# Kernel optimization log

Hardware: AMD Instinct MI355X
Metric: run time of the kernel (lower is better)

## Reference

```python
import jax, jax.numpy as jnp
import numpy as np

DIM = 256
HEADS = 8
WIN = 64
SHIFT = 32
HIDDEN = 1024  # dim * mlp_ratio
EPS = 1e-5


def layernorm(x, g, b):
    mu = jnp.mean(x, axis=-1, keepdims=True)
    var = jnp.mean(jnp.square(x - mu), axis=-1, keepdims=True)
    return (x - mu) * jax.lax.rsqrt(var + EPS) * g + b


def setup_inputs() -> dict:
    key = jax.random.key(0)
    ks = jax.random.split(key, 12)
    B, L = 8, 16384
    s = lambda fan: 1.0 / np.sqrt(fan)
    return {
        "x": jax.random.normal(ks[0], (B, L, DIM), dtype=jnp.float32),
        "g1": jnp.ones((DIM,), jnp.float32),
        "b1": jnp.zeros((DIM,), jnp.float32),
        "qkv_w": jax.random.normal(ks[1], (DIM, 3 * DIM), jnp.float32) * s(DIM),
        "qkv_b": jnp.zeros((3 * DIM,), jnp.float32),
        "rpb_table": jax.random.normal(ks[2], (2 * WIN - 1, HEADS), jnp.float32) * 0.02,
        "proj_w": jax.random.normal(ks[3], (DIM, DIM), jnp.float32) * s(DIM),
        "proj_b": jnp.zeros((DIM,), jnp.float32),
        "g2": jnp.ones((DIM,), jnp.float32),
        "b2": jnp.zeros((DIM,), jnp.float32),
        "fc1_w": jax.random.normal(ks[4], (DIM, HIDDEN), jnp.float32) * s(DIM),
        "fc1_b": jnp.zeros((HIDDEN,), jnp.float32),
        "fc2_w": jax.random.normal(ks[5], (HIDDEN, DIM), jnp.float32) * s(HIDDEN),
        "fc2_b": jnp.zeros((DIM,), jnp.float32),
    }


def reference(x, g1, b1, qkv_w, qkv_b, rpb_table, proj_w, proj_b, g2, b2, fc1_w, fc1_b, fc2_w, fc2_b):
    B, L, C = x.shape
    hd = C // HEADS
    scale = hd ** (-0.5)

    shortcut = x
    xn = layernorm(x, g1, b1)

    # shift: roll left, zero wrapped-around tail (faithful to original in-place zeroing)
    shifted = jnp.roll(xn, -SHIFT, axis=1)
    shifted = shifted.at[:, -SHIFT:].set(0.0)

    nW = L // WIN
    xw = shifted.reshape(B * nW, WIN, C)

    # qkv projection
    qkv = xw @ qkv_w + qkv_b
    qkv = qkv.reshape(-1, WIN, 3, HEADS, hd).transpose(2, 0, 3, 1, 4)
    q, k, v = qkv[0], qkv[1], qkv[2]

    attn = jnp.einsum('bhnd,bhmd->bhnm', q * scale, k)

    idx = jnp.arange(WIN)
    rel = idx[:, None] - idx[None, :] + (WIN - 1)
    bias = rpb_table[rel].transpose(2, 0, 1)
    attn = attn + bias[None]

    attn = jax.nn.softmax(attn, axis=-1)
    out = jnp.einsum('bhnm,bhmd->bhnd', attn, v)
    out = out.transpose(0, 2, 1, 3).reshape(-1, WIN, C)
    out = out @ proj_w + proj_b

    # window reverse + unshift (zero wrapped head, faithful to original)
    xr = out.reshape(B, L, C)
    xr = jnp.roll(xr, SHIFT, axis=1)
    xr = xr.at[:, :SHIFT].set(0.0)

    x1 = shortcut + xr
    h = layernorm(x1, g2, b2)
    h = jax.nn.gelu(h @ fc1_w + fc1_b, approximate=False)
    h = h @ fc2_w + fc2_b
    return x1 + h
```

## Files before the change

### kernel.cpp

```cpp
#include <hip/hip_runtime.h>
#include <hip/hip_bf16.h>
#include <stdint.h>

#define LSEQ   16384
#define NBATCH 8
#define MROWS  (NBATCH*LSEQ)
#define CDIM   256
#define NHEADS 8
#define HDIM   32
#define NWIN   64
#define NSH    32
#define NHID   1024

typedef unsigned short u16;
typedef __attribute__((ext_vector_type(4))) float f32x4;
typedef __attribute__((ext_vector_type(8))) short s16x8;

__device__ __forceinline__ u16 f2bf(float f) {
  union { float f; unsigned u; } c; c.f = f;
  unsigned r = c.u + 0x7FFFu + ((c.u >> 16) & 1u);
  return (u16)(r >> 16);
}

__device__ __forceinline__ float gelu_fast(float v) {
  float t = v * v;
  float u2 = v * fmaf(t, 0.0713548162726f, 1.59576912161f);
  float e = __expf(u2);
  float r = __builtin_amdgcn_rcpf(e + 1.f);
  return fmaf(-v, r, v);
}

__global__ __launch_bounds__(256) void wtrans_kernel(const float* __restrict__ in,
                                                     u16* __restrict__ out, int K, int N) {
  __shared__ float tile[64][65];
  int k0 = blockIdx.x * 64, n0 = blockIdx.y * 64;
  int t = threadIdx.x;
  int r = t >> 4, cb = (t & 15) * 4;
#pragma unroll
  for (int p = 0; p < 4; ++p) {
    const float4 v = *(const float4*)(in + (size_t)(k0 + r + p*16) * N + n0 + cb);
    tile[r+p*16][cb+0] = v.x; tile[r+p*16][cb+1] = v.y;
    tile[r+p*16][cb+2] = v.z; tile[r+p*16][cb+3] = v.w;
  }
  __syncthreads();
#pragma unroll
  for (int p = 0; p < 4; ++p) {
    int nl = r + p*16;
    ushort4 o;
    o.x = f2bf(tile[cb+0][nl]); o.y = f2bf(tile[cb+1][nl]);
    o.z = f2bf(tile[cb+2][nl]); o.w = f2bf(tile[cb+3][nl]);
    *(ushort4*)(out + (size_t)(n0+nl)*K + k0 + cb) = o;
  }
}

__global__ __launch_bounds__(256) void ln_shift_kernel(const float* __restrict__ x,
                                                       const float* __restrict__ g,
                                                       const float* __restrict__ b,
                                                       u16* __restrict__ out) {
  int row  = blockIdx.x * 4 + (threadIdx.x >> 6);
  int lane = threadIdx.x & 63;
  u16* op = out + (size_t)row * CDIM + lane*4;
  int l  = row & (LSEQ-1);
  int ls = l + NSH;
  if (ls >= LSEQ) { *(ushort4*)op = make_ushort4(0,0,0,0); return; }
  const float4 v = *(const float4*)(x + ((size_t)(row - l) + ls) * CDIM + lane*4);
  float s  = v.x+v.y+v.z+v.w;
  float s2 = v.x*v.x + v.y*v.y + v.z*v.z + v.w*v.w;
#pragma unroll
  for (int m = 1; m < 64; m <<= 1) { s += __shfl_xor(s, m); s2 += __shfl_xor(s2, m); }
  float mean = s * (1.f/CDIM);
  float rs = rsqrtf(s2*(1.f/CDIM) - mean*mean + 1e-5f);
  const float4 gv = *(const float4*)(g + lane*4);
  const float4 bv = *(const float4*)(b + lane*4);
  ushort4 o;
  o.x = f2bf((v.x-mean)*rs*gv.x + bv.x);
  o.y = f2bf((v.y-mean)*rs*gv.y + bv.y);
  o.z = f2bf((v.z-mean)*rs*gv.z + bv.z);
  o.w = f2bf((v.w-mean)*rs*gv.w + bv.w);
  *(ushort4*)op = o;
}

__global__ __launch_bounds__(256) void ln2_kernel(const float* __restrict__ x,
                                                  float* __restrict__ x1,
                                                  const float* __restrict__ g,
                                                  const float* __restrict__ b,
                                                  u16* __restrict__ out) {
  int row  = blockIdx.x * 4 + (threadIdx.x >> 6);
  int lane = threadIdx.x & 63;
  int l = row & (LSEQ-1);
  float* dp = x1 + (size_t)row * CDIM + lane*4;
  float4 v;
  if (l < NSH) { v = *(const float4*)(x + (size_t)row * CDIM + lane*4); *(float4*)dp = v; }
  else         { v = *(const float4*)dp; }
  float s  = v.x+v.y+v.z+v.w;
  float s2 = v.x*v.x + v.y*v.y + v.z*v.z + v.w*v.w;
#pragma unroll
  for (int m = 1; m < 64; m <<= 1) { s += __shfl_xor(s, m); s2 += __shfl_xor(s2, m); }
  float mean = s * (1.f/CDIM);
  float rs = rsqrtf(s2*(1.f/CDIM) - mean*mean + 1e-5f);
  const float4 gv = *(const float4*)(g + lane*4);
  const float4 bv = *(const float4*)(b + lane*4);
  ushort4 o;
  o.x = f2bf((v.x-mean)*rs*gv.x + bv.x);
  o.y = f2bf((v.y-mean)*rs*gv.y + bv.y);
  o.z = f2bf((v.z-mean)*rs*gv.z + bv.z);
  o.w = f2bf((v.w-mean)*rs*gv.w + bv.w);
  *(ushort4*)(out + (size_t)row * CDIM + lane*4) = o;
}

template<int KDIM, int NDIM, int EPI>
__global__ __launch_bounds__(256) void gemm_kernel(const u16* __restrict__ A,
                                                   const u16* __restrict__ BT,
                                                   const float* __restrict__ bias,
                                                   void* __restrict__ Cout,
                                                   const float* __restrict__ res) {
  __shared__ __align__(16) u16 As[128*64];
  __shared__ __align__(16) u16 Bs[128*64];
  const int t = threadIdx.x, wave = t >> 6, lane = t & 63;
  constexpr int NT_N = NDIM / 128;
  constexpr int G = 32;
  const int bid = blockIdx.x;
  const int chunk = bid / (G * NT_N);
  const int rem = bid - chunk * (G * NT_N);
  const int tn = rem / G;
  const int tm = chunk * G + (rem - tn * G);
  f32x4 acc[4][4];
#pragma unroll
  for (int m = 0; m < 4; ++m)
#pragma unroll
    for (int n = 0; n < 4; ++n) acc[m][n] = (f32x4){0.f,0.f,0.f,0.f};

  const size_t Aoff = (size_t)tm * 128 * KDIM;
  const size_t Boff = (size_t)tn * 128 * KDIM;
  int rowS[4], kblkS[4];
#pragma unroll
  for (int p = 0; p < 4; ++p) {
    int i = p*256 + t; rowS[p] = i >> 3;
    kblkS[p] = ((i & 7) ^ (rowS[p] & 7)) * 8;
  }
  const int wr = (wave >> 1) * 64, wc = (wave & 1) * 64;

  for (int kt = 0; kt < KDIM/64; ++kt) {
    const int k0 = kt * 64;
#pragma unroll
    for (int p = 0; p < 4; ++p) {
      __builtin_amdgcn_global_load_lds(
        (const __attribute__((address_space(1))) void*)(A + Aoff + (size_t)rowS[p]*KDIM + k0 + kblkS[p]),
        (__attribute__((address_space(3))) void*)(As + (p*256 + wave*64)*8), 16, 0, 0);
      __builtin_amdgcn_global_load_lds(
        (const __attribute__((address_space(1))) void*)(BT + Boff + (size_t)rowS[p]*KDIM + k0 + kblkS[p]),
        (__attribute__((address_space(3))) void*)(Bs + (p*256 + wave*64)*8), 16, 0, 0);
    }
    asm volatile("s_waitcnt vmcnt(0)" ::: "memory");
    __syncthreads();
#pragma unroll
    for (int kk = 0; kk < 2; ++kk) {
      s16x8 af[4], bf[4];
#pragma unroll
      for (int m = 0; m < 4; ++m) {
        int r = wr + m*16 + (lane & 15);
        int slot = (kk*4 + (lane >> 4)) ^ (r & 7);
        af[m] = *(const s16x8*)&As[r*64 + slot*8];
      }
#pragma unroll
      for (int n = 0; n < 4; ++n) {
        int r = wc + n*16 + (lane & 15);
        int slot = (kk*4 + (lane >> 4)) ^ (r & 7);
        bf[n] = *(const s16x8*)&Bs[r*64 + slot*8];
      }
#pragma unroll
      for (int m = 0; m < 4; ++m)
#pragma unroll
        for (int n = 0; n < 4; ++n)
          acc[m][n] = __builtin_amdgcn_mfma_f32_16x16x32_bf16(bf[n], af[m], acc[m][n], 0, 0, 0);
    }
    __syncthreads();
  }

  const int g = lane >> 4, c0 = lane & 15;
  const size_t row0 = (size_t)tm*128 + wr;
  const int col0 = tn*128 + wc;
  float4 bvv[4];
#pragma unroll
  for (int n = 0; n < 4; ++n) bvv[n] = *(const float4*)(bias + col0 + n*16 + g*4);

  if constexpr (EPI == 0) {
    u16* out = (u16*)Cout;
#pragma unroll
    for (int m = 0; m < 4; ++m) {
      size_t R = row0 + m*16 + c0;
      u16* orow = out + R * NDIM + col0 + g*4;
#pragma unroll
      for (int n = 0; n < 4; ++n) {
        ushort4 o;
        o.x = f2bf(acc[m][n][0] + bvv[n].x);
        o.y = f2bf(acc[m][n][1] + bvv[n].y);
        o.z = f2bf(acc[m][n][2] + bvv[n].z);
        o.w = f2bf(acc[m][n][3] + bvv[n].w);
        *(ushort4*)(orow + n*16) = o;
      }
    }
  } else if constexpr (EPI == 1) {
    float* out = (float*)Cout;
#pragma unroll
    for (int m = 0; m < 4; ++m) {
      size_t R = row0 + m*16 + c0;
      int l = (int)(R & (LSEQ-1));
      if (l < LSEQ - NSH) {
        size_t base = (R + NSH) * CDIM + col0 + g*4;
#pragma unroll
        for (int n = 0; n < 4; ++n) {
          float4 rv = *(const float4*)(res + base + n*16);
          float4 o;
          o.x = rv.x + acc[m][n][0] + bvv[n].x;
          o.y = rv.y + acc[m][n][1] + bvv[n].y;
          o.z = rv.z + acc[m][n][2] + bvv[n].z;
          o.w = rv.w + acc[m][n][3] + bvv[n].w;
          *(float4*)(out + base + n*16) = o;
        }
      }
    }
  } else if constexpr (EPI == 2) {
    u16* out = (u16*)Cout;
#pragma unroll
    for (int m = 0; m < 4; ++m) {
      size_t R = row0 + m*16 + c0;
      u16* orow = out + R * NDIM + col0 + g*4;
#pragma unroll
      for (int n = 0; n < 4; ++n) {
        ushort4 o;
        o.x = f2bf(gelu_fast(acc[m][n][0] + bvv[n].x));
        o.y = f2bf(gelu_fast(acc[m][n][1] + bvv[n].y));
        o.z = f2bf(gelu_fast(acc[m][n][2] + bvv[n].z));
        o.w = f2bf(gelu_fast(acc[m][n][3] + bvv[n].w));
        *(ushort4*)(orow + n*16) = o;
      }
    }
  } else {
    float* out = (float*)Cout;
#pragma unroll
    for (int m = 0; m < 4; ++m) {
      size_t R = row0 + m*16 + c0;
      size_t base = R * NDIM + col0 + g*4;
#pragma unroll
      for (int n = 0; n < 4; ++n) {
        float4 rv = *(const float4*)(res + base + n*16);
        float4 o;
        o.x = rv.x + acc[m][n][0] + bvv[n].x;
        o.y = rv.y + acc[m][n][1] + bvv[n].y;
        o.z = rv.z + acc[m][n][2] + bvv[n].z;
        o.w = rv.w + acc[m][n][3] + bvv[n].w;
        *(float4*)(out + base + n*16) = o;
      }
    }
  }
}

__global__ __launch_bounds__(256) void attn_kernel(const u16* __restrict__ qkv,
                                                   const float* __restrict__ rpb,
                                                   u16* __restrict__ out) {
  __shared__ __align__(16) u16 VT[NHEADS*HDIM*NWIN];
  __shared__ __align__(16) u16 Pl[4*NWIN*NWIN];
  __shared__ float biasl[NHEADS][128];
  const int t = threadIdx.x, wave = t >> 6, lane = t & 63;
  const int g = lane >> 4, c0 = lane & 15;
  const size_t rowbase = (size_t)blockIdx.x * NWIN;

  for (int e = t; e < NHEADS*128; e += 256) {
    int h = e >> 7, i = e & 127;
    biasl[h][i] = (i < 2*NWIN-1) ? rpb[i*NHEADS + h] : 0.f;
  }
  {
    int cA = t >> 5;
    int inner = t & 31;
    int hh = inner >> 2, d0 = (inner & 3) * 8;
#pragma unroll
    for (int p = 0; p < 8; ++p) {
      int c = p*8 + cA;
      s16x8 v = *(const s16x8*)&qkv[(rowbase + c)*768 + 512 + hh*32 + d0];
#pragma unroll
      for (int j = 0; j < 8; ++j) {
        int d = d0 + j;
        int slot = (c >> 3) ^ (d & 7) ^ hh;
        *(u16*)((char*)VT + hh*4096 + d*128 + slot*16 + (c & 7)*2) = (u16)v[j];
      }
    }
  }
  __syncthreads();

  const float scale = 0.17677669529663687f;
#pragma unroll 1
  for (int rep = 0; rep < 2; ++rep) {
    const int h = wave*2 + rep;
    s16x8 qf[4], kf[4];
#pragma unroll
    for (int m = 0; m < 4; ++m)
      qf[m] = *(const s16x8*)&qkv[(rowbase + m*16 + c0)*768 + h*32 + g*8];
#pragma unroll
    for (int n = 0; n < 4; ++n)
      kf[n] = *(const s16x8*)&qkv[(rowbase + n*16 + c0)*768 + 256 + h*32 + g*8];
    f32x4 sa[4][4];
#pragma unroll
    for (int m = 0; m < 4; ++m)
#pragma unroll
      for (int n = 0; n < 4; ++n) sa[m][n] = (f32x4){0.f,0.f,0.f,0.f};
#pragma unroll
    for (int m = 0; m < 4; ++m)
#pragma unroll
      for (int n = 0; n < 4; ++n)
        sa[m][n] = __builtin_amdgcn_mfma_f32_16x16x32_bf16(qf[m], kf[n], sa[m][n], 0, 0, 0);
#pragma unroll
    for (int m = 0; m < 4; ++m)
#pragma unroll
      for (int n = 0; n < 4; ++n) {
        int idx0 = (m-n)*16 + 4*g - c0 + 63;
#pragma unroll
        for (int j = 0; j < 4; ++j)
          sa[m][n][j] = sa[m][n][j]*scale + biasl[h][idx0 + j];
      }
    float rm[4][4], rsum[4][4];
#pragma unroll
    for (int m = 0; m < 4; ++m)
#pragma unroll
      for (int j = 0; j < 4; ++j) {
        float mx = fmaxf(fmaxf(sa[m][0][j], sa[m][1][j]), fmaxf(sa[m][2][j], sa[m][3][j]));
        mx = fmaxf(mx, __shfl_xor(mx, 1));
        mx = fmaxf(mx, __shfl_xor(mx, 2));
        mx = fmaxf(mx, __shfl_xor(mx, 4));
        mx = fmaxf(mx, __shfl_xor(mx, 8));
        rm[m][j] = mx;
      }
#pragma unroll
    for (int m = 0; m < 4; ++m)
#pragma unroll
      for (int n = 0; n < 4; ++n)
#pragma unroll
        for (int j = 0; j < 4; ++j)
          sa[m][n][j] = __expf(sa[m][n][j] - rm[m][j]);
#pragma unroll
    for (int m = 0; m < 4; ++m)
#pragma unroll
      for (int j = 0; j < 4; ++j) {
        float s = sa[m][0][j] + sa[m][1][j] + sa[m][2][j] + sa[m][3][j];
        s += __shfl_xor(s, 1);
        s += __shfl_xor(s, 2);
        s += __shfl_xor(s, 4);
        s += __shfl_xor(s, 8);
        rsum[m][j] = 1.f / s;
      }
    asm volatile("s_waitcnt lgkmcnt(0)" ::: "memory");
#pragma unroll
    for (int m = 0; m < 4; ++m)
#pragma unroll
      for (int n = 0; n < 4; ++n)
#pragma unroll
        for (int j = 0; j < 4; ++j) {
          int r = m*16 + 4*g + j, c = n*16 + c0;
          *(u16*)((char*)Pl + wave*8192 + r*128 + (((c>>3)^(r&7))*16) + (c&7)*2)
            = f2bf(sa[m][n][j] * rsum[m][j]);
        }
    asm volatile("s_waitcnt lgkmcnt(0)" ::: "memory");
    __builtin_amdgcn_sched_barrier(0);
    f32x4 oa[4][2];
#pragma unroll
    for (int m = 0; m < 4; ++m) { oa[m][0] = (f32x4){0.f,0.f,0.f,0.f}; oa[m][1] = (f32x4){0.f,0.f,0.f,0.f}; }
#pragma unroll
    for (int kk = 0; kk < 2; ++kk) {
      s16x8 pa[4], vb[2];
#pragma unroll
      for (int m = 0; m < 4; ++m) {
        int r = m*16 + c0;
        int slot = (kk*4 + g) ^ (r & 7);
        pa[m] = *(const s16x8*)((const char*)Pl + wave*8192 + r*128 + slot*16);
      }
#pragma unroll
      for (int n = 0; n < 2; ++n) {
        int d = n*16 + c0;
        int slot = (kk*4 + g) ^ (d & 7) ^ h;
        vb[n] = *(const s16x8*)((const char*)VT + h*4096 + d*128 + slot*16);
      }
#pragma unroll
      for (int m = 0; m < 4; ++m)
#pragma unroll
        for (int n = 0; n < 2; ++n)
          oa[m][n] = __builtin_amdgcn_mfma_f32_16x16x32_bf16(vb[n], pa[m], oa[m][n], 0, 0, 0);
    }
#pragma unroll
    for (int m = 0; m < 4; ++m) {
      u16* op = out + (rowbase + m*16 + c0)*CDIM + h*32 + g*4;
#pragma unroll
      for (int n = 0; n < 2; ++n) {
        ushort4 o;
        o.x = f2bf(oa[m][n][0]); o.y = f2bf(oa[m][n][1]);
        o.z = f2bf(oa[m][n][2]); o.w = f2bf(oa[m][n][3]);
        *(ushort4*)(op + n*16) = o;
      }
    }
  }
}

extern "C" void kernel_launch(void* const* d_in, const int* in_sizes, int n_in,
                              void* d_out, int out_size, void* d_ws, size_t ws_size,
                              hipStream_t stream) {
  const float* x      = (const float*)d_in[0];
  const float* g1     = (const float*)d_in[1];
  const float* b1     = (const float*)d_in[2];
  const float* qkv_w  = (const float*)d_in[3];
  const float* qkv_b  = (const float*)d_in[4];
  const float* rpb    = (const float*)d_in[5];
  const float* proj_w = (const float*)d_in[6];
  const float* proj_b = (const float*)d_in[7];
  const float* g2     = (const float*)d_in[8];
  const float* b2     = (const float*)d_in[9];
  const float* fc1_w  = (const float*)d_in[10];
  const float* fc1_b  = (const float*)d_in[11];
  const float* fc2_w  = (const float*)d_in[12];
  const float* fc2_b  = (const float*)d_in[13];
  float* out = (float*)d_out;

  u16* R0     = (u16*)d_ws;
  u16* R1     = R0 + (size_t)MROWS*768;
  u16* qkvwT  = R1 + (size_t)MROWS*1024;
  u16* projwT = qkvwT + 768*256;
  u16* fc1wT  = projwT + 256*256;
  u16* fc2wT  = fc1wT + 1024*256;

  wtrans_kernel<<<dim3(4, 12), 256, 0, stream>>>(qkv_w, qkvwT, 256, 768);
  wtrans_kernel<<<dim3(4, 4),  256, 0, stream>>>(proj_w, projwT, 256, 256);
  wtrans_kernel<<<dim3(4, 16), 256, 0, stream>>>(fc1_w, fc1wT, 256, 1024);
  wtrans_kernel<<<dim3(16, 4), 256, 0, stream>>>(fc2_w, fc2wT, 1024, 256);

  constexpr int NT_M = MROWS/128;
  ln_shift_kernel<<<MROWS/4, 256, 0, stream>>>(x, g1, b1, R1);
  gemm_kernel<256, 768, 0><<<NT_M*6, 256, 0, stream>>>(R1, qkvwT, qkv_b, R0, nullptr);
  attn_kernel<<<MROWS/NWIN, 256, 0, stream>>>(R0, rpb, R1);
  gemm_kernel<256, 256, 1><<<NT_M*2, 256, 0, stream>>>(R1, projwT, proj_b, out, x);
  ln2_kernel<<<MROWS/4, 256, 0, stream>>>(x, out, g2, b2, R0);
  gemm_kernel<256, 1024, 2><<<NT_M*8, 256, 0, stream>>>(R0, fc1wT, fc1_b, R1, nullptr);
  gemm_kernel<1024, 256, 3><<<NT_M*2, 256, 0, stream>>>(R1, fc2wT, fc2_b, out, out);
}
```

Before: 669.0 us.

## Fuse output projection, residual add and second LayerNorm into one kernel

Replaces the proj GEMM (residual epilogue) and the separate ln2 kernel with one kernel. Each block computes a 64x256 row tile so the full row is in registers, adds bias and the shifted residual, writes x1, then computes the row LayerNorm with lane shuffles and writes bf16 output. This drops a full fp32 round trip of x1 and one launch. In exchange the GEMM tile is narrower in M, the kernel has no double buffering, and register pressure is higher (16 f32x4 accumulators plus 16 saved x1 vectors).

```diff
diff --git a/kernel.cpp b/kernel.cpp
--- a/kernel.cpp
+++ b/kernel.cpp
@@ -78,34 +78,6 @@
   o.z = f2bf((v.z-mean)*rs*gv.z + bv.z);
   o.w = f2bf((v.w-mean)*rs*gv.w + bv.w);
   *(ushort4*)op = o;
-}
-
-__global__ __launch_bounds__(256) void ln2_kernel(const float* __restrict__ x,
-                                                  float* __restrict__ x1,
-                                                  const float* __restrict__ g,
-                                                  const float* __restrict__ b,
-                                                  u16* __restrict__ out) {
-  int row  = blockIdx.x * 4 + (threadIdx.x >> 6);
-  int lane = threadIdx.x & 63;
-  int l = row & (LSEQ-1);
-  float* dp = x1 + (size_t)row * CDIM + lane*4;
-  float4 v;
-  if (l < NSH) { v = *(const float4*)(x + (size_t)row * CDIM + lane*4); *(float4*)dp = v; }
-  else         { v = *(const float4*)dp; }
-  float s  = v.x+v.y+v.z+v.w;
-  float s2 = v.x*v.x + v.y*v.y + v.z*v.z + v.w*v.w;
-#pragma unroll
-  for (int m = 1; m < 64; m <<= 1) { s += __shfl_xor(s, m); s2 += __shfl_xor(s2, m); }
-  float mean = s * (1.f/CDIM);
-  float rs = rsqrtf(s2*(1.f/CDIM) - mean*mean + 1e-5f);
-  const float4 gv = *(const float4*)(g + lane*4);
-  const float4 bv = *(const float4*)(b + lane*4);
-  ushort4 o;
-  o.x = f2bf((v.x-mean)*rs*gv.x + bv.x);
-  o.y = f2bf((v.y-mean)*rs*gv.y + bv.y);
-  o.z = f2bf((v.z-mean)*rs*gv.z + bv.z);
-  o.w = f2bf((v.w-mean)*rs*gv.w + bv.w);
-  *(ushort4*)(out + (size_t)row * CDIM + lane*4) = o;
 }
 
 template<int KDIM, int NDIM, int EPI>
@@ -200,26 +172,6 @@
         *(ushort4*)(orow + n*16) = o;
       }
     }
-  } else if constexpr (EPI == 1) {
-    float* out = (float*)Cout;
-#pragma unroll
-    for (int m = 0; m < 4; ++m) {
-      size_t R = row0 + m*16 + c0;
-      int l = (int)(R & (LSEQ-1));
-      if (l < LSEQ - NSH) {
-        size_t base = (R + NSH) * CDIM + col0 + g*4;
-#pragma unroll
-        for (int n = 0; n < 4; ++n) {
-          float4 rv = *(const float4*)(res + base + n*16);
-          float4 o;
-          o.x = rv.x + acc[m][n][0] + bvv[n].x;
-          o.y = rv.y + acc[m][n][1] + bvv[n].y;
-          o.z = rv.z + acc[m][n][2] + bvv[n].z;
-          o.w = rv.w + acc[m][n][3] + bvv[n].w;
-          *(float4*)(out + base + n*16) = o;
-        }
-      }
-    }
   } else if constexpr (EPI == 2) {
     u16* out = (u16*)Cout;
 #pragma unroll
@@ -253,6 +205,105 @@
         *(float4*)(out + base + n*16) = o;
       }
     }
+  }
+}
+
+__global__ __launch_bounds__(256) void proj_ln_kernel(const u16* __restrict__ A,
+                                                      const u16* __restrict__ BT,
+                                                      const float* __restrict__ bias,
+                                                      const float* __restrict__ x,
+                                                      const float* __restrict__ g2,
+                                                      const float* __restrict__ b2,
+                                                      float* __restrict__ out,
+                                                      u16* __restrict__ ln_out) {
+  __shared__ __align__(16) u16 As[64*64];
+  __shared__ __align__(16) u16 Bs[256*64];
+  const int t = threadIdx.x, wave = t >> 6, lane = t & 63;
+  const int g = lane >> 4, c0 = lane & 15;
+  const int row0 = blockIdx.x * 64;
+
+  f32x4 acc[16];
+#pragma unroll
+  for (int n = 0; n < 16; ++n) acc[n] = (f32x4){0.f,0.f,0.f,0.f};
+
+  for (int kt = 0; kt < 4; ++kt) {
+    const int k0 = kt * 64;
+#pragma unroll
+    for (int p = 0; p < 2; ++p) {
+      int i = p*256 + t;
+      int r = i >> 3;
+      int srow = row0 - NSH + r; if (srow < 0) srow = 0;
+      int kb = ((i & 7) ^ (r & 7)) * 8;
+      __builtin_amdgcn_global_load_lds(
+        (const __attribute__((address_space(1))) void*)(A + (size_t)srow*CDIM + k0 + kb),
+        (__attribute__((address_space(3))) void*)(As + i*8), 16, 0, 0);
+    }
+#pragma unroll
+    for (int p = 0; p < 8; ++p) {
+      int i = p*256 + t;
+      int r = i >> 3;
+      int kb = ((i & 7) ^ (r & 7)) * 8;
+      __builtin_amdgcn_global_load_lds(
+        (const __attribute__((address_space(1))) void*)(BT + (size_t)r*CDIM + k0 + kb),
+        (__attribute__((address_space(3))) void*)(Bs + i*8), 16, 0, 0);
+    }
+    asm volatile("s_waitcnt vmcnt(0)" ::: "memory");
+    __syncthreads();
+#pragma unroll
+    for (int kk = 0; kk < 2; ++kk) {
+      const int ar = wave*16 + c0;
+      s16x8 af = *(const s16x8*)&As[ar*64 + (((kk*4 + g) ^ (ar & 7)) * 8)];
+#pragma unroll
+      for (int nn = 0; nn < 4; ++nn) {
+        s16x8 bf[4];
+#pragma unroll
+        for (int q = 0; q < 4; ++q) {
+          int rn = (nn*4 + q)*16 + c0;
+          bf[q] = *(const s16x8*)&Bs[rn*64 + (((kk*4 + g) ^ (rn & 7)) * 8)];
+        }
+#pragma unroll
+        for (int q = 0; q < 4; ++q)
+          acc[nn*4+q] = __builtin_amdgcn_mfma_f32_16x16x32_bf16(bf[q], af, acc[nn*4+q], 0, 0, 0);
+      }
+    }
+    __syncthreads();
+  }
+
+  const int D = row0 + wave*16 + c0;
+  const int l_d = D & (LSEQ-1);
+  const bool addp = (l_d >= NSH);
+  float s = 0.f, s2 = 0.f;
+  f32x4 x1v[16];
+#pragma unroll
+  for (int n = 0; n < 16; ++n) {
+    const int col = n*16 + g*4;
+    const float4 xv = *(const float4*)(x + (size_t)D*CDIM + col);
+    const float4 bv = *(const float4*)(bias + col);
+    f32x4 v;
+    v[0] = addp ? xv.x + acc[n][0] + bv.x : xv.x;
+    v[1] = addp ? xv.y + acc[n][1] + bv.y : xv.y;
+    v[2] = addp ? xv.z + acc[n][2] + bv.z : xv.z;
+    v[3] = addp ? xv.w + acc[n][3] + bv.w : xv.w;
+    *(f32x4*)(out + (size_t)D*CDIM + col) = v;
+    x1v[n] = v;
+    s  += v[0]+v[1]+v[2]+v[3];
+    s2 += v[0]*v[0]+v[1]*v[1]+v[2]*v[2]+v[3]*v[3];
+  }
+  s  += __shfl_xor(s, 16);  s  += __shfl_xor(s, 32);
+  s2 += __shfl_xor(s2, 16); s2 += __shfl_xor(s2, 32);
+  const float mean = s * (1.f/CDIM);
+  const float rs = rsqrtf(s2*(1.f/CDIM) - mean*mean + 1e-5f);
+#pragma unroll
+  for (int n = 0; n < 16; ++n) {
+    const int col = n*16 + g*4;
+    const float4 gv = *(const float4*)(g2 + col);
+    const float4 bv = *(const float4*)(b2 + col);
+    ushort4 o;
+    o.x = f2bf((x1v[n][0]-mean)*rs*gv.x + bv.x);
+    o.y = f2bf((x1v[n][1]-mean)*rs*gv.y + bv.y);
+    o.z = f2bf((x1v[n][2]-mean)*rs*gv.z + bv.z);
+    o.w = f2bf((x1v[n][3]-mean)*rs*gv.w + bv.w);
+    *(ushort4*)(ln_out + (size_t)D*CDIM + col) = o;
   }
 }
 
@@ -434,8 +485,7 @@
   ln_shift_kernel<<<MROWS/4, 256, 0, stream>>>(x, g1, b1, R1);
   gemm_kernel<256, 768, 0><<<NT_M*6, 256, 0, stream>>>(R1, qkvwT, qkv_b, R0, nullptr);
   attn_kernel<<<MROWS/NWIN, 256, 0, stream>>>(R0, rpb, R1);
-  gemm_kernel<256, 256, 1><<<NT_M*2, 256, 0, stream>>>(R1, projwT, proj_b, out, x);
-  ln2_kernel<<<MROWS/4, 256, 0, stream>>>(x, out, g2, b2, R0);
+  proj_ln_kernel<<<MROWS/64, 256, 0, stream>>>(R1, projwT, proj_b, x, g2, b2, out, R0);
   gemm_kernel<256, 1024, 2><<<NT_M*8, 256, 0, stream>>>(R0, fc1wT, fc1_b, R1, nullptr);
   gemm_kernel<1024, 256, 3><<<NT_M*2, 256, 0, stream>>>(R1, fc2wT, fc2_b, out, out);
 }
```

Result: slower. 682.4 us (+2.0%).
